# Performance work log

Hardware: AMD Instinct MI355X
Metric: run time of the kernel (lower is better)

## Reference

```python
import jax, jax.numpy as jnp
import numpy as np

B, S, H, I, E, TOP_K = 16, 2048, 768, 3072, 8, 2


def setup_inputs() -> dict:
    key = jax.random.key(0)
    ks = jax.random.split(key, 5)
    scaled = lambda k, shape, fan_in: jax.random.normal(k, shape, jnp.float32) * (fan_in ** -0.5)
    return {
        "hidden_states": jax.random.normal(ks[0], (B, S, H), jnp.float32),
        "gate_w": scaled(ks[1], (E, H), H),          # router: nn.Linear(H, E, bias=False)
        "w1": scaled(ks[2], (E, H, I), H),            # expert intermediate.dense
        "b1": jnp.zeros((E, I), jnp.float32),
        "w2": scaled(ks[3], (E, I, H), I),            # expert output.dense
        "b2": jnp.zeros((E, H), jnp.float32),
    }


def reference(hidden_states, gate_w, w1, b1, w2, b2):
    b, s, h = hidden_states.shape
    e = gate_w.shape[0]
    x = hidden_states.reshape(-1, h)  # [T, H], T = B*S
    # Router
    router_logits = x @ gate_w.T  # [T, E]
    probs = jax.nn.softmax(router_logits.astype(jnp.float32), axis=-1)
    rw, sel = jax.lax.top_k(probs, TOP_K)  # [T, top_k]
    rw = rw / rw.sum(axis=-1, keepdims=True)
    rw = rw.astype(x.dtype)
    # Dense combine weights: zero for unselected experts (equivalent to the
    # gather/index_add dispatch in the torch code, full-capacity no-drop MoE).
    combine = (jax.nn.one_hot(sel, e, dtype=x.dtype) * rw[..., None]).sum(axis=1)  # [T, E]
    out = jnp.zeros_like(x)
    for ei in range(e):  # fixed small expert loop
        hmid = jax.nn.gelu(x @ w1[ei] + b1[ei], approximate=False)  # [T, I]
        y = hmid @ w2[ei] + b2[ei]  # [T, H] (dropout is identity in eval)
        out = out + combine[:, ei:ei + 1] * y
    return out.reshape(b, s, h), router_logits
```

## Files before the change

### kernel.cpp

```cpp
#include <hip/hip_runtime.h>
#include <hip/hip_bf16.h>
#include <math.h>
#include <stdint.h>

#define T_TOK 32768
#define H_DIM 768
#define I_DIM 3072
#define E_NUM 8
#define PADROWS 66560
#define NTILE   520

typedef __attribute__((ext_vector_type(8))) __bf16 bf16x8;
typedef __attribute__((ext_vector_type(4))) float floatx4;

__device__ inline __bf16 f2bf(float f) { return (__bf16)f; }
__device__ inline unsigned short f2bfu(float f) {
    __bf16 b = (__bf16)f; return *(unsigned short*)&b;
}

__device__ inline void g2lds16(const void* g, void* l) {
    __builtin_amdgcn_global_load_lds(
        (const __attribute__((address_space(1))) unsigned int*)g,
        (__attribute__((address_space(3))) unsigned int*)l, 16, 0, 0);
}

__device__ inline float gelu_fast(float x) {
    float x2 = x * x;
    float t = x * (0.7978845608f + 0.0356774081f * x2);
    float e = __expf(-2.f * t);
    return x / (1.f + e);
}

__global__ __launch_bounds__(256) void router_kernel(
    const float* __restrict__ x, const float* __restrict__ gw,
    float* __restrict__ logits, int* __restrict__ tok_sel,
    float* __restrict__ tok_w, int* __restrict__ cnt)
{
    __shared__ float sgw[E_NUM * H_DIM];
    __shared__ int lcnt[E_NUM];
    int tid = threadIdx.x;
    for (int i = tid; i < E_NUM * H_DIM; i += 256) sgw[i] = gw[i];
    if (tid < E_NUM) lcnt[tid] = 0;
    __syncthreads();

    int t = blockIdx.x * 256 + tid;
    const float* xr = x + (size_t)t * H_DIM;
    float acc[E_NUM];
#pragma unroll
    for (int e = 0; e < E_NUM; e++) acc[e] = 0.f;
    for (int k = 0; k < H_DIM; k += 4) {
        float4 xv = *(const float4*)(xr + k);
#pragma unroll
        for (int e = 0; e < E_NUM; e++) {
            const float* g = &sgw[e * H_DIM + k];
            acc[e] += xv.x * g[0] + xv.y * g[1] + xv.z * g[2] + xv.w * g[3];
        }
    }
#pragma unroll
    for (int e = 0; e < E_NUM; e++) logits[(size_t)t * E_NUM + e] = acc[e];

    int e1 = 0; float v1 = acc[0];
#pragma unroll
    for (int e = 1; e < E_NUM; e++) if (acc[e] > v1) { v1 = acc[e]; e1 = e; }
    int e2 = (e1 == 0) ? 1 : 0; float v2 = acc[(e1 == 0) ? 1 : 0];
#pragma unroll
    for (int e = 0; e < E_NUM; e++)
        if (e != e1 && acc[e] > v2) { v2 = acc[e]; e2 = e; }

    float p2 = expf(v2 - v1);
    float s = 1.f + p2;
    tok_sel[2 * t] = e1; tok_sel[2 * t + 1] = e2;
    tok_w[2 * t] = 1.f / s; tok_w[2 * t + 1] = p2 / s;

    atomicAdd(&lcnt[e1], 1); atomicAdd(&lcnt[e2], 1);
    __syncthreads();
    if (tid < E_NUM) atomicAdd(&cnt[tid], lcnt[tid]);
}

__global__ void scan_kernel(const int* __restrict__ cnt, int* __restrict__ off)
{
    if (threadIdx.x == 0 && blockIdx.x == 0) {
        int o = 0;
        for (int e = 0; e < E_NUM; e++) {
            off[e] = o;
            o += (cnt[e] + 127) & ~127;
        }
        off[E_NUM] = o;
    }
}

__global__ __launch_bounds__(256) void scatter_kernel(
    const int* __restrict__ tok_sel, const float* __restrict__ tok_w,
    const int* __restrict__ off, int* __restrict__ fill,
    int* __restrict__ pair_token, float* __restrict__ pair_w)
{
    __shared__ int lcnt[E_NUM];
    __shared__ int base[E_NUM];
    int tid = threadIdx.x;
    if (tid < E_NUM) lcnt[tid] = 0;
    __syncthreads();
    int t = blockIdx.x * 256 + tid;
    int e1 = tok_sel[2 * t], e2 = tok_sel[2 * t + 1];
    int lp1 = atomicAdd(&lcnt[e1], 1);
    int lp2 = atomicAdd(&lcnt[e2], 1);
    __syncthreads();
    if (tid < E_NUM) base[tid] = (lcnt[tid] > 0) ? atomicAdd(&fill[tid], lcnt[tid]) : 0;
    __syncthreads();
    int p1 = off[e1] + base[e1] + lp1;
    int p2 = off[e2] + base[e2] + lp2;
    pair_token[p1] = t; pair_w[p1] = tok_w[2 * t];
    pair_token[p2] = t; pair_w[p2] = tok_w[2 * t + 1];
}

__global__ __launch_bounds__(256) void convert_x(
    const float* __restrict__ x, __bf16* __restrict__ xb)
{
    int i = blockIdx.x * 256 + threadIdx.x;
    float4 a = ((const float4*)x)[2 * i];
    float4 b = ((const float4*)x)[2 * i + 1];
    bf16x8 o;
    o[0] = f2bf(a.x); o[1] = f2bf(a.y); o[2] = f2bf(a.z); o[3] = f2bf(a.w);
    o[4] = f2bf(b.x); o[5] = f2bf(b.y); o[6] = f2bf(b.z); o[7] = f2bf(b.w);
    ((bf16x8*)xb)[i] = o;
}

__global__ __launch_bounds__(256) void transpose_w(
    const float* __restrict__ W, __bf16* __restrict__ Wt, int R, int C)
{
    __shared__ unsigned short T[64][66];
    int e = blockIdx.z;
    int r0 = blockIdx.y * 64, c0 = blockIdx.x * 64;
    const float* Wp = W + (size_t)e * R * C;
    __bf16* Wtp = Wt + (size_t)e * C * R;
    int tid = threadIdx.x;

    int rl = tid >> 2, cg = tid & 3;
    const float* src = Wp + (size_t)(r0 + rl) * C + c0 + cg * 16;
#pragma unroll
    for (int u = 0; u < 4; u++) {
        float4 v = *(const float4*)(src + u * 4);
        unsigned p0 = (unsigned)f2bfu(v.x) | ((unsigned)f2bfu(v.y) << 16);
        unsigned p1 = (unsigned)f2bfu(v.z) | ((unsigned)f2bfu(v.w) << 16);
        *(unsigned*)&T[rl][cg * 16 + u * 4]     = p0;
        *(unsigned*)&T[rl][cg * 16 + u * 4 + 2] = p1;
    }
    __syncthreads();

    int cl = tid >> 2, rg = tid & 3;
    __bf16* dst = Wtp + (size_t)(c0 + cl) * R + r0 + rg * 16;
#pragma unroll
    for (int half = 0; half < 2; half++) {
        bf16x8 o;
#pragma unroll
        for (int j = 0; j < 8; j++) {
            unsigned short b = T[rg * 16 + half * 8 + j][cl];
            o[j] = *(__bf16*)&b;
        }
        *(bf16x8*)(dst + half * 8) = o;
    }
}

__global__ __launch_bounds__(256) void moe_gemm1(
    const __bf16* __restrict__ xbf, const __bf16* __restrict__ w1t,
    const float* __restrict__ b1, const int* __restrict__ off_g,
    const int* __restrict__ pair_token, __bf16* __restrict__ hmid,
    int chunk_base, int chunkI)
{
    __shared__ __align__(16) __bf16 As[128][32];
    __shared__ __align__(16) __bf16 Bs[128][32];
    int m0 = blockIdx.x * 128;
    if (m0 >= off_g[E_NUM]) return;
    int e = 0;
#pragma unroll
    for (int k = 0; k < E_NUM - 1; k++) if (m0 >= off_g[k + 1]) e = k + 1;

    int tid = threadIdx.x;
    int w = tid >> 6, lane = tid & 63;
    int ln = lane & 15, q = lane >> 4;
    int wm = w >> 1, wn = w & 1;
    int sub = lane >> 2, kp = lane & 3;
    int i0 = chunk_base + blockIdx.y * 128;

    int rA0 = m0 + w * 32 + sub;
    int t0 = pair_token[rA0]; if (t0 < 0) t0 = 0;
    int t1 = pair_token[rA0 + 16]; if (t1 < 0) t1 = 0;
    const __bf16* gA0 = xbf + (size_t)t0 * H_DIM + kp * 8;
    const __bf16* gA1 = xbf + (size_t)t1 * H_DIM + kp * 8;
    const __bf16* gB0 = w1t + ((size_t)e * I_DIM + i0 + w * 32 + sub) * H_DIM + kp * 8;
    const __bf16* gB1 = gB0 + (size_t)16 * H_DIM;
    void* lA0 = &As[w * 32][0];
    void* lA1 = &As[w * 32 + 16][0];
    void* lB0 = &Bs[w * 32][0];
    void* lB1 = &Bs[w * 32 + 16][0];

    floatx4 acc[4][4];
#pragma unroll
    for (int a = 0; a < 4; a++)
#pragma unroll
        for (int b = 0; b < 4; b++) acc[a][b] = (floatx4){0.f, 0.f, 0.f, 0.f};

    for (int kk = 0; kk < H_DIM; kk += 32) {
        __syncthreads();
        g2lds16(gA0 + kk, lA0);
        g2lds16(gA1 + kk, lA1);
        g2lds16(gB0 + kk, lB0);
        g2lds16(gB1 + kk, lB1);
        __syncthreads();
        bf16x8 af[4], bfr[4];
#pragma unroll
        for (int mt = 0; mt < 4; mt++) af[mt] = *(bf16x8*)&As[wm * 64 + mt * 16 + ln][q * 8];
#pragma unroll
        for (int nt = 0; nt < 4; nt++) bfr[nt] = *(bf16x8*)&Bs[wn * 64 + nt * 16 + ln][q * 8];
#pragma unroll
        for (int mt = 0; mt < 4; mt++)
#pragma unroll
            for (int nt = 0; nt < 4; nt++)
                acc[mt][nt] = __builtin_amdgcn_mfma_f32_16x16x32_bf16(af[mt], bfr[nt], acc[mt][nt], 0, 0, 0);
    }

#pragma unroll
    for (int nt = 0; nt < 4; nt++) {
        int colg = i0 + wn * 64 + nt * 16 + ln;
        float bv = b1[e * I_DIM + colg];
        int coll = colg - chunk_base;
#pragma unroll
        for (int mt = 0; mt < 4; mt++)
#pragma unroll
            for (int r = 0; r < 4; r++) {
                int row = m0 + wm * 64 + mt * 16 + q * 4 + r;
                float v = acc[mt][nt][r] + bv;
                hmid[(size_t)row * chunkI + coll] = f2bf(gelu_fast(v));
            }
    }
}

__global__ __launch_bounds__(256) void moe_gemm2(
    const __bf16* __restrict__ hmid, const __bf16* __restrict__ w2t,
    const float* __restrict__ b2, const int* __restrict__ off_g,
    const int* __restrict__ pair_token, const float* __restrict__ pair_w,
    float* __restrict__ out, int chunk_base, int chunkI)
{
    __shared__ __align__(16) __bf16 As[128][32];
    __shared__ __align__(16) __bf16 Bs[128][32];
    int m0 = blockIdx.x * 128;
    if (m0 >= off_g[E_NUM]) return;
    int e = 0;
#pragma unroll
    for (int k = 0; k < E_NUM - 1; k++) if (m0 >= off_g[k + 1]) e = k + 1;

    int tid = threadIdx.x;
    int w = tid >> 6, lane = tid & 63;
    int ln = lane & 15, q = lane >> 4;
    int wm = w >> 1, wn = w & 1;
    int sub = lane >> 2, kp = lane & 3;
    int h0 = blockIdx.y * 128;

    const __bf16* gA0 = hmid + (size_t)(m0 + w * 32 + sub) * chunkI + kp * 8;
    const __bf16* gA1 = gA0 + (size_t)16 * chunkI;
    const __bf16* gB0 = w2t + ((size_t)e * H_DIM + h0 + w * 32 + sub) * I_DIM + chunk_base + kp * 8;
    const __bf16* gB1 = gB0 + (size_t)16 * I_DIM;
    void* lA0 = &As[w * 32][0];
    void* lA1 = &As[w * 32 + 16][0];
    void* lB0 = &Bs[w * 32][0];
    void* lB1 = &Bs[w * 32 + 16][0];

    floatx4 acc[4][4];
#pragma unroll
    for (int a = 0; a < 4; a++)
#pragma unroll
        for (int b = 0; b < 4; b++) acc[a][b] = (floatx4){0.f, 0.f, 0.f, 0.f};

    for (int kk = 0; kk < chunkI; kk += 32) {
        __syncthreads();
        g2lds16(gA0 + kk, lA0);
        g2lds16(gA1 + kk, lA1);
        g2lds16(gB0 + kk, lB0);
        g2lds16(gB1 + kk, lB1);
        __syncthreads();
        bf16x8 af[4], bfr[4];
#pragma unroll
        for (int mt = 0; mt < 4; mt++) af[mt] = *(bf16x8*)&As[wm * 64 + mt * 16 + ln][q * 8];
#pragma unroll
        for (int nt = 0; nt < 4; nt++) bfr[nt] = *(bf16x8*)&Bs[wn * 64 + nt * 16 + ln][q * 8];
#pragma unroll
        for (int mt = 0; mt < 4; mt++)
#pragma unroll
            for (int nt = 0; nt < 4; nt++)
                acc[mt][nt] = __builtin_amdgcn_mfma_f32_16x16x32_bf16(af[mt], bfr[nt], acc[mt][nt], 0, 0, 0);
    }

    float bv[4];
#pragma unroll
    for (int nt = 0; nt < 4; nt++) bv[nt] = b2[e * H_DIM + h0 + wn * 64 + nt * 16 + ln];

#pragma unroll
    for (int mt = 0; mt < 4; mt++)
#pragma unroll
        for (int r = 0; r < 4; r++) {
            int row = m0 + wm * 64 + mt * 16 + q * 4 + r;
            int tok = pair_token[row];
            if (tok < 0) continue;
            float pw = pair_w[row];
            float* orow = out + (size_t)tok * H_DIM + h0 + wn * 64;
#pragma unroll
            for (int nt = 0; nt < 4; nt++) {
                float v = (acc[mt][nt][r] + bv[nt]) * pw;
                atomicAdd(orow + nt * 16 + ln, v);
            }
        }
}

extern "C" void kernel_launch(void* const* d_in, const int* in_sizes, int n_in,
                              void* d_out, int out_size, void* d_ws, size_t ws_size,
                              hipStream_t stream)
{
    const float* x  = (const float*)d_in[0];
    const float* gw = (const float*)d_in[1];
    const float* w1 = (const float*)d_in[2];
    const float* b1 = (const float*)d_in[3];
    const float* w2 = (const float*)d_in[4];
    const float* b2 = (const float*)d_in[5];
    float* out = (float*)d_out;
    float* logits = out + (size_t)T_TOK * H_DIM;

    char* p0 = (char*)d_ws;
    char* p = p0;
    int* cnt  = (int*)p; p += 32;
    int* fill = (int*)p; p += 32;
    int* off  = (int*)p; p += 64;
    int* tok_sel = (int*)p;  p += (size_t)2 * T_TOK * 4;
    float* tok_w = (float*)p; p += (size_t)2 * T_TOK * 4;
    int* pair_token = (int*)p;  p += (size_t)PADROWS * 4;
    float* pair_w   = (float*)p; p += (size_t)PADROWS * 4;
    p = (char*)(((uintptr_t)p + 255) & ~(uintptr_t)255);
    __bf16* xbf = (__bf16*)p; p += (size_t)T_TOK * H_DIM * 2;
    __bf16* w1t = (__bf16*)p; p += (size_t)E_NUM * H_DIM * I_DIM * 2;
    __bf16* w2t = (__bf16*)p; p += (size_t)E_NUM * H_DIM * I_DIM * 2;
    p = (char*)(((uintptr_t)p + 255) & ~(uintptr_t)255);
    __bf16* hmid = (__bf16*)p;
    size_t used = (size_t)(p - p0);
    size_t avail = (ws_size > used) ? ws_size - used : 0;

    static const int cands[] = {3072, 1536, 1024, 768, 512, 384, 256, 128};
    int chunkI = 128;
    for (int i = 0; i < 8; i++)
        if ((size_t)PADROWS * (size_t)cands[i] * 2 <= avail) { chunkI = cands[i]; break; }

    hipMemsetAsync(out, 0, (size_t)T_TOK * H_DIM * sizeof(float), stream);
    hipMemsetAsync(cnt, 0, 128, stream);
    hipMemsetAsync(pair_token, 0xFF, (size_t)PADROWS * 4, stream);

    convert_x<<<(T_TOK * H_DIM / 8) / 256, 256, 0, stream>>>(x, xbf);
    transpose_w<<<dim3(I_DIM / 64, H_DIM / 64, E_NUM), 256, 0, stream>>>(w1, w1t, H_DIM, I_DIM);
    transpose_w<<<dim3(H_DIM / 64, I_DIM / 64, E_NUM), 256, 0, stream>>>(w2, w2t, I_DIM, H_DIM);

    router_kernel<<<T_TOK / 256, 256, 0, stream>>>(x, gw, logits, tok_sel, tok_w, cnt);
    scan_kernel<<<1, 64, 0, stream>>>(cnt, off);
    scatter_kernel<<<T_TOK / 256, 256, 0, stream>>>(tok_sel, tok_w, off, fill,
                                                    pair_token, pair_w);

    for (int cb = 0; cb < I_DIM; cb += chunkI) {
        moe_gemm1<<<dim3(NTILE, chunkI / 128), 256, 0, stream>>>(
            xbf, w1t, b1, off, pair_token, hmid, cb, chunkI);
        moe_gemm2<<<dim3(NTILE, H_DIM / 128), 256, 0, stream>>>(
            hmid, w2t, b2, off, pair_token, pair_w, out, cb, chunkI);
    }
}
```

Measured before the change: 1.698 ms.

## Replace atomic scatter-add with per-pair bf16 outputs and a gather combine

When workspace allows, the second expert GEMM writes each routed pair's output as bf16 into a pair-indexed buffer instead of atomically adding into the fp32 output. A new combine kernel then gathers each token's two rows through recorded positions, adds the biases, weights them and writes the result once, so the output memset is no longer needed. The GEMMs are row-chunked across the full intermediate dimension rather than chunked over I. The old atomic path is kept as a fallback, now adding the bias only on the first chunk so it is not added repeatedly. Rounding the expert outputs to bf16 costs some precision, and the extra pair buffer adds memory traffic.

```diff
diff --git a/kernel.cpp b/kernel.cpp
--- a/kernel.cpp
+++ b/kernel.cpp
@@ -17,6 +17,9 @@
 __device__ inline unsigned short f2bfu(float f) {
     __bf16 b = (__bf16)f; return *(unsigned short*)&b;
 }
+__device__ inline float bfu2f(unsigned short u) {
+    union { unsigned v; float f; } c; c.v = ((unsigned)u) << 16; return c.f;
+}
 
 __device__ inline void g2lds16(const void* g, void* l) {
     __builtin_amdgcn_global_load_lds(
@@ -92,7 +95,8 @@
 __global__ __launch_bounds__(256) void scatter_kernel(
     const int* __restrict__ tok_sel, const float* __restrict__ tok_w,
     const int* __restrict__ off, int* __restrict__ fill,
-    int* __restrict__ pair_token, float* __restrict__ pair_w)
+    int* __restrict__ pair_token, float* __restrict__ pair_w,
+    int* __restrict__ tok_pos)
 {
     __shared__ int lcnt[E_NUM];
     __shared__ int base[E_NUM];
@@ -110,6 +114,7 @@
     int p2 = off[e2] + base[e2] + lp2;
     pair_token[p1] = t; pair_w[p1] = tok_w[2 * t];
     pair_token[p2] = t; pair_w[p2] = tok_w[2 * t + 1];
+    tok_pos[2 * t] = p1; tok_pos[2 * t + 1] = p2;
 }
 
 __global__ __launch_bounds__(256) void convert_x(
@@ -164,11 +169,11 @@
     const __bf16* __restrict__ xbf, const __bf16* __restrict__ w1t,
     const float* __restrict__ b1, const int* __restrict__ off_g,
     const int* __restrict__ pair_token, __bf16* __restrict__ hmid,
-    int chunk_base, int chunkI)
+    int chunk_base, int chunkI, int r0)
 {
     __shared__ __align__(16) __bf16 As[128][32];
     __shared__ __align__(16) __bf16 Bs[128][32];
-    int m0 = blockIdx.x * 128;
+    int m0 = r0 + blockIdx.x * 128;
     if (m0 >= off_g[E_NUM]) return;
     int e = 0;
 #pragma unroll
@@ -229,12 +234,100 @@
             for (int r = 0; r < 4; r++) {
                 int row = m0 + wm * 64 + mt * 16 + q * 4 + r;
                 float v = acc[mt][nt][r] + bv;
-                hmid[(size_t)row * chunkI + coll] = f2bf(gelu_fast(v));
+                hmid[(size_t)(row - r0) * chunkI + coll] = f2bf(gelu_fast(v));
             }
     }
 }
 
-__global__ __launch_bounds__(256) void moe_gemm2(
+__global__ __launch_bounds__(256) void moe_gemm2_y(
+    const __bf16* __restrict__ hmid, const __bf16* __restrict__ w2t,
+    const int* __restrict__ off_g, __bf16* __restrict__ y_pair, int r0)
+{
+    __shared__ __align__(16) __bf16 As[128][32];
+    __shared__ __align__(16) __bf16 Bs[128][32];
+    int m0 = r0 + blockIdx.x * 128;
+    if (m0 >= off_g[E_NUM]) return;
+    int e = 0;
+#pragma unroll
+    for (int k = 0; k < E_NUM - 1; k++) if (m0 >= off_g[k + 1]) e = k + 1;
+
+    int tid = threadIdx.x;
+    int w = tid >> 6, lane = tid & 63;
+    int ln = lane & 15, q = lane >> 4;
+    int wm = w >> 1, wn = w & 1;
+    int sub = lane >> 2, kp = lane & 3;
+    int h0 = blockIdx.y * 128;
+
+    const __bf16* gA0 = hmid + (size_t)(m0 - r0 + w * 32 + sub) * I_DIM + kp * 8;
+    const __bf16* gA1 = gA0 + (size_t)16 * I_DIM;
+    const __bf16* gB0 = w2t + ((size_t)e * H_DIM + h0 + w * 32 + sub) * I_DIM + kp * 8;
+    const __bf16* gB1 = gB0 + (size_t)16 * I_DIM;
+    void* lA0 = &As[w * 32][0];
+    void* lA1 = &As[w * 32 + 16][0];
+    void* lB0 = &Bs[w * 32][0];
+    void* lB1 = &Bs[w * 32 + 16][0];
+
+    floatx4 acc[4][4];
+#pragma unroll
+    for (int a = 0; a < 4; a++)
+#pragma unroll
+        for (int b = 0; b < 4; b++) acc[a][b] = (floatx4){0.f, 0.f, 0.f, 0.f};
+
+    for (int kk = 0; kk < I_DIM; kk += 32) {
+        __syncthreads();
+        g2lds16(gA0 + kk, lA0);
+        g2lds16(gA1 + kk, lA1);
+        g2lds16(gB0 + kk, lB0);
+        g2lds16(gB1 + kk, lB1);
+        __syncthreads();
+        bf16x8 af[4], bfr[4];
+#pragma unroll
+        for (int mt = 0; mt < 4; mt++) af[mt] = *(bf16x8*)&As[wm * 64 + mt * 16 + ln][q * 8];
+#pragma unroll
+        for (int nt = 0; nt < 4; nt++) bfr[nt] = *(bf16x8*)&Bs[wn * 64 + nt * 16 + ln][q * 8];
+#pragma unroll
+        for (int mt = 0; mt < 4; mt++)
+#pragma unroll
+            for (int nt = 0; nt < 4; nt++)
+                acc[mt][nt] = __builtin_amdgcn_mfma_f32_16x16x32_bf16(af[mt], bfr[nt], acc[mt][nt], 0, 0, 0);
+    }
+
+#pragma unroll
+    for (int mt = 0; mt < 4; mt++)
+#pragma unroll
+        for (int r = 0; r < 4; r++) {
+            int row = m0 + wm * 64 + mt * 16 + q * 4 + r;
+            __bf16* yrow = y_pair + (size_t)row * H_DIM + h0 + wn * 64;
+#pragma unroll
+            for (int nt = 0; nt < 4; nt++)
+                yrow[nt * 16 + ln] = f2bf(acc[mt][nt][r]);
+        }
+}
+
+__global__ __launch_bounds__(256) void combine_kernel(
+    const __bf16* __restrict__ y_pair, const int* __restrict__ tok_pos,
+    const int* __restrict__ tok_sel, const float* __restrict__ tok_w,
+    const float* __restrict__ b2, float* __restrict__ out)
+{
+    int g = blockIdx.x * 256 + threadIdx.x;
+    int t = g / 192;
+    int u = g - t * 192;
+    int p1 = tok_pos[2 * t], p2 = tok_pos[2 * t + 1];
+    int e1 = tok_sel[2 * t], e2 = tok_sel[2 * t + 1];
+    float w1 = tok_w[2 * t], w2 = tok_w[2 * t + 1];
+    ushort4 a = *(const ushort4*)(y_pair + (size_t)p1 * H_DIM + u * 4);
+    ushort4 b = *(const ushort4*)(y_pair + (size_t)p2 * H_DIM + u * 4);
+    float4 ba = *(const float4*)(b2 + e1 * H_DIM + u * 4);
+    float4 bb = *(const float4*)(b2 + e2 * H_DIM + u * 4);
+    float4 o;
+    o.x = w1 * (bfu2f(a.x) + ba.x) + w2 * (bfu2f(b.x) + bb.x);
+    o.y = w1 * (bfu2f(a.y) + ba.y) + w2 * (bfu2f(b.y) + bb.y);
+    o.z = w1 * (bfu2f(a.z) + ba.z) + w2 * (bfu2f(b.z) + bb.z);
+    o.w = w1 * (bfu2f(a.w) + ba.w) + w2 * (bfu2f(b.w) + bb.w);
+    *(float4*)(out + (size_t)t * H_DIM + u * 4) = o;
+}
+
+__global__ __launch_bounds__(256) void moe_gemm2_atomic(
     const __bf16* __restrict__ hmid, const __bf16* __restrict__ w2t,
     const float* __restrict__ b2, const int* __restrict__ off_g,
     const int* __restrict__ pair_token, const float* __restrict__ pair_w,
@@ -289,9 +382,10 @@
                 acc[mt][nt] = __builtin_amdgcn_mfma_f32_16x16x32_bf16(af[mt], bfr[nt], acc[mt][nt], 0, 0, 0);
     }
 
+    float bscale = (chunk_base == 0) ? 1.f : 0.f;
     float bv[4];
 #pragma unroll
-    for (int nt = 0; nt < 4; nt++) bv[nt] = b2[e * H_DIM + h0 + wn * 64 + nt * 16 + ln];
+    for (int nt = 0; nt < 4; nt++) bv[nt] = bscale * b2[e * H_DIM + h0 + wn * 64 + nt * 16 + ln];
 
 #pragma unroll
     for (int mt = 0; mt < 4; mt++)
@@ -323,6 +417,11 @@
     float* out = (float*)d_out;
     float* logits = out + (size_t)T_TOK * H_DIM;
 
+    const size_t XBF_SZ = (size_t)T_TOK * H_DIM * 2;
+    const size_t W1T_SZ = (size_t)E_NUM * H_DIM * I_DIM * 2;
+    const size_t W2T_SZ = W1T_SZ;
+    const size_t YP_SZ  = (size_t)PADROWS * H_DIM * 2;
+
     char* p0 = (char*)d_ws;
     char* p = p0;
     int* cnt  = (int*)p; p += 32;
@@ -330,39 +429,67 @@
     int* off  = (int*)p; p += 64;
     int* tok_sel = (int*)p;  p += (size_t)2 * T_TOK * 4;
     float* tok_w = (float*)p; p += (size_t)2 * T_TOK * 4;
+    int* tok_pos = (int*)p;  p += (size_t)2 * T_TOK * 4;
     int* pair_token = (int*)p;  p += (size_t)PADROWS * 4;
     float* pair_w   = (float*)p; p += (size_t)PADROWS * 4;
     p = (char*)(((uintptr_t)p + 255) & ~(uintptr_t)255);
-    __bf16* xbf = (__bf16*)p; p += (size_t)T_TOK * H_DIM * 2;
-    __bf16* w1t = (__bf16*)p; p += (size_t)E_NUM * H_DIM * I_DIM * 2;
-    __bf16* w2t = (__bf16*)p; p += (size_t)E_NUM * H_DIM * I_DIM * 2;
-    p = (char*)(((uintptr_t)p + 255) & ~(uintptr_t)255);
-    __bf16* hmid = (__bf16*)p;
-    size_t used = (size_t)(p - p0);
-    size_t avail = (ws_size > used) ? ws_size - used : 0;
-
-    static const int cands[] = {3072, 1536, 1024, 768, 512, 384, 256, 128};
-    int chunkI = 128;
-    for (int i = 0; i < 8; i++)
-        if ((size_t)PADROWS * (size_t)cands[i] * 2 <= avail) { chunkI = cands[i]; break; }
-
-    hipMemsetAsync(out, 0, (size_t)T_TOK * H_DIM * sizeof(float), stream);
+
+    __bf16* xbf = (__bf16*)p;
+    __bf16* w1t = (__bf16*)(p + XBF_SZ);
+    __bf16* w2t = (__bf16*)(p + XBF_SZ + W1T_SZ);
+    char* after_w = p + XBF_SZ + W1T_SZ + W2T_SZ;
+
+    size_t base_fused = (size_t)(after_w - p0) + YP_SZ;
+    long long avail_f = (long long)ws_size - (long long)base_fused;
+    int mrows = 0;
+    if (avail_f >= (long long)128 * I_DIM * 2) {
+        long long r = avail_f / ((long long)I_DIM * 2);
+        if (r > PADROWS) r = PADROWS;
+        mrows = (int)(r & ~127LL);
+    }
+    bool fused = (mrows >= 128);
+
     hipMemsetAsync(cnt, 0, 128, stream);
     hipMemsetAsync(pair_token, 0xFF, (size_t)PADROWS * 4, stream);
+
+    router_kernel<<<T_TOK / 256, 256, 0, stream>>>(x, gw, logits, tok_sel, tok_w, cnt);
+    scan_kernel<<<1, 64, 0, stream>>>(cnt, off);
+    scatter_kernel<<<T_TOK / 256, 256, 0, stream>>>(tok_sel, tok_w, off, fill,
+                                                    pair_token, pair_w, tok_pos);
 
     convert_x<<<(T_TOK * H_DIM / 8) / 256, 256, 0, stream>>>(x, xbf);
     transpose_w<<<dim3(I_DIM / 64, H_DIM / 64, E_NUM), 256, 0, stream>>>(w1, w1t, H_DIM, I_DIM);
     transpose_w<<<dim3(H_DIM / 64, I_DIM / 64, E_NUM), 256, 0, stream>>>(w2, w2t, I_DIM, H_DIM);
 
-    router_kernel<<<T_TOK / 256, 256, 0, stream>>>(x, gw, logits, tok_sel, tok_w, cnt);
-    scan_kernel<<<1, 64, 0, stream>>>(cnt, off);
-    scatter_kernel<<<T_TOK / 256, 256, 0, stream>>>(tok_sel, tok_w, off, fill,
-                                                    pair_token, pair_w);
-
-    for (int cb = 0; cb < I_DIM; cb += chunkI) {
-        moe_gemm1<<<dim3(NTILE, chunkI / 128), 256, 0, stream>>>(
-            xbf, w1t, b1, off, pair_token, hmid, cb, chunkI);
-        moe_gemm2<<<dim3(NTILE, H_DIM / 128), 256, 0, stream>>>(
-            hmid, w2t, b2, off, pair_token, pair_w, out, cb, chunkI);
-    }
-}
+    if (fused) {
+        __bf16* y_pair = (__bf16*)after_w;
+        __bf16* hmid = (__bf16*)(after_w + YP_SZ);
+
+        for (int r0 = 0; r0 < PADROWS; r0 += mrows) {
+            int rows = PADROWS - r0; if (rows > mrows) rows = mrows;
+            int xt = rows / 128;
+            moe_gemm1<<<dim3(xt, I_DIM / 128), 256, 0, stream>>>(
+                xbf, w1t, b1, off, pair_token, hmid, 0, I_DIM, r0);
+            moe_gemm2_y<<<dim3(xt, H_DIM / 128), 256, 0, stream>>>(
+                hmid, w2t, off, y_pair, r0);
+        }
+        combine_kernel<<<(T_TOK * 192) / 256, 256, 0, stream>>>(
+            y_pair, tok_pos, tok_sel, tok_w, b2, out);
+    } else {
+        char* hm = after_w;
+        size_t avail = (ws_size > (size_t)(hm - p0)) ? ws_size - (size_t)(hm - p0) : 0;
+        static const int cands[] = {3072, 1536, 1024, 768, 512, 384, 256, 128};
+        int chunkI = 128;
+        for (int i = 0; i < 8; i++)
+            if ((size_t)PADROWS * (size_t)cands[i] * 2 <= avail) { chunkI = cands[i]; break; }
+        __bf16* hmid = (__bf16*)hm;
+
+        hipMemsetAsync(out, 0, (size_t)T_TOK * H_DIM * sizeof(float), stream);
+        for (int cb = 0; cb < I_DIM; cb += chunkI) {
+            moe_gemm1<<<dim3(NTILE, chunkI / 128), 256, 0, stream>>>(
+                xbf, w1t, b1, off, pair_token, hmid, cb, chunkI, 0);
+            moe_gemm2_atomic<<<dim3(NTILE, H_DIM / 128), 256, 0, stream>>>(
+                hmid, w2t, b2, off, pair_token, pair_w, out, cb, chunkI);
+        }
+    }
+}
```

Measured after the change: 1.494 ms. 12.0% less time.
